# Optimization experiments

Hardware: AMD Instinct MI355X
Metric: run time of the kernel (lower is better)

Reference implementation:

```python
import jax, jax.numpy as jnp
import numpy as np

B, DIM1, DIM2, LATENT, T = 16, 1024, 1024, 512, 2048  # T == video_feat_dim
LN_EPS = 1e-5


def setup_inputs() -> dict:
    key = jax.random.key(0)
    ks = jax.random.split(key, 8)
    def xavier(k, shape):
        fan_out, fan_in = shape
        std = float(np.sqrt(2.0 / (fan_in + fan_out)))
        return jax.random.normal(k, shape, dtype=jnp.float32) * std
    return {
        "input1": jax.random.normal(ks[0], (B, DIM1, T), dtype=jnp.float32),
        "input2": jax.random.normal(ks[1], (B, DIM2, T), dtype=jnp.float32),
        "theta_w": xavier(ks[2], (LATENT, DIM2)),
        "theta_b": jnp.zeros((LATENT,), jnp.float32),
        "phi_w": xavier(ks[3], (LATENT, DIM1)),
        "phi_b": jnp.zeros((LATENT,), jnp.float32),
        "g_w": xavier(ks[4], (LATENT, DIM1)),
        "g_b": jnp.zeros((LATENT,), jnp.float32),
        "ln_gamma": jnp.ones((LATENT, T), jnp.float32),
        "ln_beta": jnp.zeros((LATENT, T), jnp.float32),
        "out_w": xavier(ks[5], (DIM2, LATENT)),
        "out_b": jnp.zeros((DIM2,), jnp.float32),
    }


def reference(input1, input2, theta_w, theta_b, phi_w, phi_b, g_w, g_b,
              ln_gamma, ln_beta, out_w, out_b):
    # 1x1 Conv1d == channel-wise matmul
    theta_x = jnp.einsum('ld,bdt->btl', theta_w, input2) + theta_b          # [B,T2,L]
    phi_x = jnp.einsum('ld,bdt->blt', phi_w, input1) + phi_b[:, None]       # [B,L,T1]
    scores = jnp.einsum('btl,bls->bts', theta_x, phi_x)                      # [B,T2,T1] (unscaled)
    p = jax.nn.softmax(scores, axis=-1)
    g_x = jnp.einsum('ld,bdt->btl', g_w, input1) + g_b                       # [B,T1,L]
    t_x = jnp.einsum('bts,bsl->blt', p, g_x)                                 # [B,L,T2]
    # LayerNorm over the last two dims jointly [LATENT, T]
    mu = jnp.mean(t_x, axis=(1, 2), keepdims=True)
    var = jnp.var(t_x, axis=(1, 2), keepdims=True)
    h = (t_x - mu) * jax.lax.rsqrt(var + LN_EPS) * ln_gamma + ln_beta
    h = jax.nn.relu(h)
    w_t = jnp.einsum('ol,blt->bot', out_w, h) + out_b[None, :, None]         # [B,DIM2,T2]
    return w_t + input2
```

## Files before the change

### kernel.cpp

```cpp
#include <hip/hip_runtime.h>
#include <hip/hip_bf16.h>

#define BB 16
#define D1 1024
#define D2 1024
#define LL 512
#define TT 2048
#define LN_EPS 1e-5f

typedef unsigned short u16;
typedef __attribute__((ext_vector_type(8))) _Float16 half8;
typedef __attribute__((ext_vector_type(4))) float f32x4;
typedef __attribute__((ext_vector_type(4))) unsigned int u32x4;

__device__ __forceinline__ u16 f2h(float v) {
    _Float16 h = (_Float16)v;
    return *(u16*)&h;
}
__device__ __forceinline__ float h2f(u16 u) {
    return (float)(*(const _Float16*)&u);
}

__device__ __forceinline__ void gload_lds16(const void* g, void* l) {
    __builtin_amdgcn_global_load_lds((const __attribute__((address_space(1))) void*)g,
                                     (__attribute__((address_space(3))) void*)l, 16, 0, 0);
}

#define MEMFENCE asm volatile("" ::: "memory")
__device__ __forceinline__ void block_barrier() {
    MEMFENCE; __builtin_amdgcn_s_barrier(); MEMFENCE;
}

template<int BIAS, int OMODE>
__global__ __launch_bounds__(512, 1) void nt_gemm(
    const u16* __restrict__ A, const u16* __restrict__ B,
    long sAb, long sBb, long sCb,
    int N, int Kd, int gx, int gy,
    const float* __restrict__ bias,
    void* __restrict__ out0,
    const float* __restrict__ resid, long sRb)
{
    __shared__ __align__(16) u16 smem[65536];

    const int nwg = gridDim.x;
    const int id = blockIdx.x;
    const int swz = (id & 7) * (nwg >> 3) + (id >> 3);
    const int bx = swz % gx;
    const int byz = swz / gx;
    const int by = byz % gy;
    const int b = byz / gy;

    const int tid = threadIdx.x;
    const long arow0 = (long)by * 256;
    const long brow0 = (long)bx * 256;
    const u16* Ab = A + (long)b * sAb + arow0 * Kd;
    const u16* Bb = B + (long)b * sBb + brow0 * Kd;

    const int wave = tid >> 6, lane = tid & 63;
    const int mh = wave >> 2;
    const int wm = mh * 128;
    const int wn = (wave & 3) * 64;
    const int lm = lane & 15, kg = lane >> 4;

    const int ntile = Kd >> 6;

    auto STAGE = [&](int buf, long k0) {
        u16* Ad = smem + buf * 32768;
        u16* Bd = Ad + 16384;
#pragma unroll
        for (int sw = 0; sw < 4; ++sw) {
            int idx = sw * 512 + tid;
            int m = idx >> 3, s = idx & 7;
            int gs = s ^ (m & 7);
            gload_lds16(Ab + k0 + (long)m * Kd + gs * 8, Ad + idx * 8);
        }
#pragma unroll
        for (int sw = 0; sw < 4; ++sw) {
            int idx = sw * 512 + tid;
            int m = idx >> 3, s = idx & 7;
            int gs = s ^ (m & 7);
            gload_lds16(Bb + k0 + (long)m * Kd + gs * 8, Bd + idx * 8);
        }
    };

    f32x4 acc[8][4];
#pragma unroll
    for (int i = 0; i < 8; ++i)
#pragma unroll
        for (int j = 0; j < 4; ++j) acc[i][j] = (f32x4){0.f, 0.f, 0.f, 0.f};

    STAGE(0, 0);
    if (ntile > 1) STAGE(1, 64);

    half8 a_[4][2], b_[2][2];

#define LOADA(ms_) do { \
    _Pragma("unroll") for (int f = 0; f < 4; ++f) \
    _Pragma("unroll") for (int kf = 0; kf < 2; ++kf) { \
        int mr = wm + (ms_) * 64 + f * 16 + lm; \
        int ss = (kf * 4 + kg) ^ (mr & 7); \
        a_[f][kf] = *(const half8*)(Ac + mr * 64 + ss * 8); } } while (0)
#define LOADB(ns_) do { \
    _Pragma("unroll") for (int f = 0; f < 2; ++f) \
    _Pragma("unroll") for (int kf = 0; kf < 2; ++kf) { \
        int nr = wn + (ns_) * 32 + f * 16 + lm; \
        int ss = (kf * 4 + kg) ^ (nr & 7); \
        b_[f][kf] = *(const half8*)(Bc + nr * 64 + ss * 8); } } while (0)
#define PH_MFMA(ms_, ns_) do { \
    block_barrier(); \
    asm volatile("s_waitcnt lgkmcnt(0)" ::: "memory"); \
    __builtin_amdgcn_sched_barrier(0); \
    __builtin_amdgcn_s_setprio(1); \
    _Pragma("unroll") for (int i = 0; i < 4; ++i) \
    _Pragma("unroll") for (int j = 0; j < 2; ++j) \
    _Pragma("unroll") for (int kf = 0; kf < 2; ++kf) \
        acc[(ms_) * 4 + i][(ns_) * 2 + j] = __builtin_amdgcn_mfma_f32_16x16x32_f16( \
            a_[i][kf], b_[j][kf], acc[(ms_) * 4 + i][(ns_) * 2 + j], 0, 0, 0); \
    __builtin_amdgcn_s_setprio(0); \
    block_barrier(); \
} while (0)

    for (int t = 0; t < ntile; ++t) {
        const int c = t & 1;
        const u16* Ac = smem + c * 32768;
        const u16* Bc = Ac + 16384;
        if (t + 1 < ntile) { asm volatile("s_waitcnt vmcnt(8)" ::: "memory"); }
        else               { asm volatile("s_waitcnt vmcnt(0)" ::: "memory"); }
        block_barrier();

        LOADA(0); LOADB(0); PH_MFMA(0, 0);
        LOADA(1);           PH_MFMA(1, 0);
        LOADB(1);           PH_MFMA(1, 1);
        LOADA(0);           PH_MFMA(0, 1);

        if (t + 2 < ntile) STAGE(c, (long)(t + 2) * 64);
    }
#undef LOADA
#undef LOADB
#undef PH_MFMA

    float* Cs = (float*)smem;
#pragma unroll
    for (int p = 0; p < 2; ++p) {
        __syncthreads();
        if (mh == p) {
#pragma unroll
            for (int ms = 0; ms < 2; ++ms)
#pragma unroll
                for (int i = 0; i < 4; ++i)
#pragma unroll
                    for (int ns = 0; ns < 2; ++ns)
#pragma unroll
                        for (int j = 0; j < 2; ++j)
#pragma unroll
                            for (int r = 0; r < 4; ++r) {
                                int row = ms * 64 + i * 16 + kg * 4 + r;
                                int col = wn + ns * 32 + j * 16 + lm;
                                Cs[row * 256 + (col ^ ((row & 7) << 2))] = acc[ms * 4 + i][ns * 2 + j][r];
                            }
        }
        __syncthreads();
        if (OMODE == 0 || OMODE == 3) {
#pragma unroll
            for (int it = 0; it < 16; ++it) {
                int elem = it * 512 + tid;
                int row = elem >> 6, c4 = elem & 63;
                int grow = (int)arow0 + p * 128 + row;
                int gcol = (int)brow0 + c4 * 4;
                f32x4 v = *(const f32x4*)&Cs[row * 256 + ((c4 ^ (row & 7)) << 2)];
                if (BIAS == 1) v += bias[grow];
                if (BIAS == 2) v += *(const f32x4*)(bias + gcol);
                long off = (long)b * sCb + (long)grow * N + gcol;
                if (OMODE == 3) {
                    f32x4 rv = __builtin_nontemporal_load(
                        (const f32x4*)(resid + (long)b * sRb + (long)grow * N + gcol));
                    v += rv;
                    __builtin_nontemporal_store(v, (f32x4*)((float*)out0 + off));
                } else {
                    *(f32x4*)((float*)out0 + off) = v;
                }
            }
        } else {
#pragma unroll
            for (int it = 0; it < 8; ++it) {
                int elem = it * 512 + tid;
                int row = elem >> 5, c8 = elem & 31;
                int grow = (int)arow0 + p * 128 + row;
                int gcol = (int)brow0 + c8 * 8;
                int g0 = (c8 * 2) ^ (row & 7);
                int g1 = (c8 * 2 + 1) ^ (row & 7);
                f32x4 u0 = *(const f32x4*)&Cs[row * 256 + g0 * 4];
                f32x4 u1 = *(const f32x4*)&Cs[row * 256 + g1 * 4];
                float vv[8] = {u0.x, u0.y, u0.z, u0.w, u1.x, u1.y, u1.z, u1.w};
                if (BIAS == 1) {
                    float bb = bias[grow];
#pragma unroll
                    for (int q = 0; q < 8; ++q) vv[q] += bb;
                }
                if (BIAS == 2) {
#pragma unroll
                    for (int q = 0; q < 8; ++q) vv[q] += bias[gcol + q];
                }
                union { u16 u[8]; u32x4 v4; } pk;
#pragma unroll
                for (int q = 0; q < 8; ++q) pk.u[q] = f2h(vv[q]);
                long off = (long)b * sCb + (long)grow * N + gcol;
                *(u32x4*)((u16*)out0 + off) = pk.v4;
            }
        }
    }
}

__device__ __forceinline__ void stage_tile_sm(const u16* __restrict__ g, int ldk, u16* lds, int tid) {
#pragma unroll
    for (int it = 0; it < 4; ++it) {
        int idx = it * 256 + tid;
        int m = idx >> 3, s = idx & 7;
        int gs = s ^ (m & 7);
        gload_lds16(g + (long)m * ldk + gs * 8, lds + idx * 8);
    }
}

template<int BIAS, int OMODE>
__global__ __launch_bounds__(256, 4) void nt_gemm_sm(
    const u16* __restrict__ A, const u16* __restrict__ B,
    long sAb, long sBb, long sCb,
    int N, int Kd, int gx, int gy,
    const float* __restrict__ bias,
    void* __restrict__ out0,
    const float* __restrict__ resid, long sRb)
{
    __shared__ __align__(16) u16 smem[2 * 128 * 64];
    u16* As = smem;
    u16* Bs = smem + 128 * 64;

    const int nwg = gridDim.x;
    const int id = blockIdx.x;
    const int swz = (id & 7) * (nwg >> 3) + (id >> 3);
    const int bx = swz % gx;
    const int byz = swz / gx;
    const int by = byz % gy;
    const int b = byz / gy;

    const int tid = threadIdx.x;
    const long arow0 = (long)by * 128;
    const long brow0 = (long)bx * 128;
    const u16* Ab = A + (long)b * sAb + arow0 * Kd;
    const u16* Bb = B + (long)b * sBb + brow0 * Kd;

    const int wave = tid >> 6, lane = tid & 63;
    const int wm = (wave >> 1) * 64, wn = (wave & 1) * 64;
    const int lm = lane & 15, kg = lane >> 4;

    f32x4 acc[4][4];
#pragma unroll
    for (int i = 0; i < 4; ++i)
#pragma unroll
        for (int j = 0; j < 4; ++j) acc[i][j] = (f32x4){0.f, 0.f, 0.f, 0.f};

    for (int k0 = 0; k0 < Kd; k0 += 64) {
        stage_tile_sm(Ab + k0, Kd, As, tid);
        stage_tile_sm(Bb + k0, Kd, Bs, tid);
        __syncthreads();
#pragma unroll
        for (int ks = 0; ks < 2; ++ks) {
            half8 af[4], bf[4];
#pragma unroll
            for (int f = 0; f < 4; ++f) {
                int mr = wm + f * 16 + lm;
                int as_ = (ks * 4 + kg) ^ (mr & 7);
                af[f] = *(const half8*)(As + mr * 64 + as_ * 8);
                int nr = wn + f * 16 + lm;
                int bs_ = (ks * 4 + kg) ^ (nr & 7);
                bf[f] = *(const half8*)(Bs + nr * 64 + bs_ * 8);
            }
#pragma unroll
            for (int i = 0; i < 4; ++i)
#pragma unroll
                for (int j = 0; j < 4; ++j)
                    acc[i][j] = __builtin_amdgcn_mfma_f32_16x16x32_f16(af[i], bf[j], acc[i][j], 0, 0, 0);
        }
        __syncthreads();
    }

    float* Cs = (float*)smem;
#pragma unroll
    for (int p = 0; p < 2; ++p) {
        if (p) __syncthreads();
        if (wm == p * 64) {
#pragma unroll
            for (int i = 0; i < 4; ++i)
#pragma unroll
                for (int j = 0; j < 4; ++j)
#pragma unroll
                    for (int r = 0; r < 4; ++r) {
                        int row = i * 16 + kg * 4 + r;
                        int col = wn + j * 16 + lm;
                        Cs[row * 128 + (col ^ ((row & 7) << 2))] = acc[i][j][r];
                    }
        }
        __syncthreads();
        if (OMODE == 0 || OMODE == 3) {
#pragma unroll
            for (int rr = 0; rr < 8; ++rr) {
                int elem = rr * 256 + tid;
                int row = elem >> 5, c4 = elem & 31;
                int grow = (int)arow0 + p * 64 + row;
                int gcol = (int)brow0 + c4 * 4;
                f32x4 v = *(const f32x4*)&Cs[row * 128 + ((c4 ^ (row & 7)) << 2)];
                if (BIAS == 1) v += bias[grow];
                if (BIAS == 2) v += *(const f32x4*)(bias + gcol);
                long off = (long)b * sCb + (long)grow * N + gcol;
                if (OMODE == 3) {
                    f32x4 rv = __builtin_nontemporal_load(
                        (const f32x4*)(resid + (long)b * sRb + (long)grow * N + gcol));
                    v += rv;
                    __builtin_nontemporal_store(v, (f32x4*)((float*)out0 + off));
                } else {
                    *(f32x4*)((float*)out0 + off) = v;
                }
            }
        } else {
#pragma unroll
            for (int rr = 0; rr < 4; ++rr) {
                int elem = rr * 256 + tid;
                int row = elem >> 4, c8 = elem & 15;
                int grow = (int)arow0 + p * 64 + row;
                int gcol = (int)brow0 + c8 * 8;
                int g0 = (c8 * 2) ^ (row & 7);
                int g1 = (c8 * 2 + 1) ^ (row & 7);
                f32x4 u0 = *(const f32x4*)&Cs[row * 128 + g0 * 4];
                f32x4 u1 = *(const f32x4*)&Cs[row * 128 + g1 * 4];
                float vv[8] = {u0.x, u0.y, u0.z, u0.w, u1.x, u1.y, u1.z, u1.w};
                if (BIAS == 1) {
                    float bb = bias[grow];
#pragma unroll
                    for (int q = 0; q < 8; ++q) vv[q] += bb;
                }
                if (BIAS == 2) {
#pragma unroll
                    for (int q = 0; q < 8; ++q) vv[q] += bias[gcol + q];
                }
                union { u16 u[8]; u32x4 v4; } pk;
#pragma unroll
                for (int q = 0; q < 8; ++q) pk.u[q] = f2h(vv[q]);
                long off = (long)b * sCb + (long)grow * N + gcol;
                *(u32x4*)((u16*)out0 + off) = pk.v4;
            }
        }
    }
}

__global__ __launch_bounds__(256) void transpose_h(const float* __restrict__ in,
                                                   u16* __restrict__ o16, int D, int T) {
    __shared__ float tile[64][65];
    int b = blockIdx.z;
    const float* src = in + (long)b * D * T;
    long obase = (long)b * D * T;
    int t0 = blockIdx.x * 64, d0 = blockIdx.y * 64;
    int tx = threadIdx.x & 63, ty = threadIdx.x >> 6;
#pragma unroll
    for (int i = 0; i < 64; i += 4)
        tile[ty + i][tx] = __builtin_nontemporal_load(&src[(long)(d0 + ty + i) * T + t0 + tx]);
    __syncthreads();
#pragma unroll
    for (int i = 0; i < 64; i += 4) {
        long o = obase + (long)(t0 + ty + i) * D + d0 + tx;
        o16[o] = f2h(tile[tx][ty + i]);
    }
}

__global__ __launch_bounds__(256) void transpose_f32(const float* __restrict__ in,
                                                     float* __restrict__ out, int R, int C) {
    __shared__ float tile[64][65];
    int c0 = blockIdx.x * 64, r0 = blockIdx.y * 64;
    int tx = threadIdx.x & 63, ty = threadIdx.x >> 6;
#pragma unroll
    for (int i = 0; i < 64; i += 4)
        tile[ty + i][tx] = in[(long)(r0 + ty + i) * C + c0 + tx];
    __syncthreads();
#pragma unroll
    for (int i = 0; i < 64; i += 4)
        out[(long)(c0 + ty + i) * R + r0 + tx] = tile[tx][ty + i];
}

__global__ __launch_bounds__(256) void conv_w(const float* __restrict__ w,
                                              u16* __restrict__ h, int n) {
    int i = blockIdx.x * 256 + threadIdx.x;
    if (i < n) h[i] = f2h(w[i]);
}

__global__ __launch_bounds__(256) void softmax_rows(const float* __restrict__ S, u16* __restrict__ P) {
    long row = (long)blockIdx.z * TT + blockIdx.x;
    const float* s = S + row * TT;
    u16* p = P + row * TT;
    int tid = threadIdx.x;
    f32x4 v0 = *(const f32x4*)(s + tid * 8);
    f32x4 v1 = *(const f32x4*)(s + tid * 8 + 4);
    float x[8] = {v0.x, v0.y, v0.z, v0.w, v1.x, v1.y, v1.z, v1.w};
    float m = x[0];
#pragma unroll
    for (int j = 1; j < 8; ++j) m = fmaxf(m, x[j]);
#pragma unroll
    for (int off = 32; off; off >>= 1) m = fmaxf(m, __shfl_xor(m, off, 64));
    __shared__ float red[8];
    int wave = tid >> 6, lane = tid & 63;
    if (lane == 0) red[wave] = m;
    __syncthreads();
    m = fmaxf(fmaxf(red[0], red[1]), fmaxf(red[2], red[3]));
    float e[8]; float sum = 0.f;
#pragma unroll
    for (int j = 0; j < 8; ++j) { e[j] = __expf(x[j] - m); sum += e[j]; }
#pragma unroll
    for (int off = 32; off; off >>= 1) sum += __shfl_xor(sum, off, 64);
    if (lane == 0) red[4 + wave] = sum;
    __syncthreads();
    sum = red[4] + red[5] + red[6] + red[7];
    float inv = 1.f / sum;
    union { u16 u[8]; u32x4 v4; } pk;
#pragma unroll
    for (int j = 0; j < 8; ++j) pk.u[j] = f2h(e[j] * inv);
    *(u32x4*)(p + tid * 8) = pk.v4;
}

__global__ void zero32(float* p) { p[threadIdx.x] = 0.f; }

__global__ __launch_bounds__(256) void ln_partial(const u16* __restrict__ TXp, float* __restrict__ sums) {
    int b = blockIdx.z;
    const u16* x = TXp + (long)b * (LL * TT) + (long)blockIdx.x * 32768;
    int tid = threadIdx.x;
    float s = 0.f, sq = 0.f;
#pragma unroll 4
    for (int j = 0; j < 16; ++j) {
        u32x4 v = *(const u32x4*)(x + (j * 256 + tid) * 8);
        unsigned w[4] = {v.x, v.y, v.z, v.w};
#pragma unroll
        for (int q = 0; q < 4; ++q) {
            float a = h2f((u16)(w[q] & 0xffff));
            float c = h2f((u16)(w[q] >> 16));
            s += a + c;
            sq += a * a + c * c;
        }
    }
#pragma unroll
    for (int off = 32; off; off >>= 1) { s += __shfl_xor(s, off, 64); sq += __shfl_xor(sq, off, 64); }
    __shared__ float rs[8];
    int wave = tid >> 6, lane = tid & 63;
    if (lane == 0) { rs[wave] = s; rs[4 + wave] = sq; }
    __syncthreads();
    if (tid == 0) {
        atomicAdd(&sums[b * 2], rs[0] + rs[1] + rs[2] + rs[3]);
        atomicAdd(&sums[b * 2 + 1], rs[4] + rs[5] + rs[6] + rs[7]);
    }
}

__global__ __launch_bounds__(256) void ln_apply(const u16* __restrict__ TXp, const float* __restrict__ sums,
                                                const float* __restrict__ gT, const float* __restrict__ bT,
                                                u16* __restrict__ H) {
    int b = blockIdx.z;
    const float n = (float)(LL * TT);
    float mu = sums[b * 2] / n;
    float var = sums[b * 2 + 1] / n - mu * mu;
    float rstd = rsqrtf(var + LN_EPS);
    long base = (long)b * (LL * TT);
    long idx = ((long)blockIdx.x * 256 + threadIdx.x) * 8;
    u32x4 xv = *(const u32x4*)(TXp + base + idx);
    unsigned w[4] = {xv.x, xv.y, xv.z, xv.w};
    f32x4 g0 = *(const f32x4*)(gT + idx);
    f32x4 g1 = *(const f32x4*)(gT + idx + 4);
    f32x4 b0 = *(const f32x4*)(bT + idx);
    f32x4 b1 = *(const f32x4*)(bT + idx + 4);
    float g[8] = {g0.x, g0.y, g0.z, g0.w, g1.x, g1.y, g1.z, g1.w};
    float be[8] = {b0.x, b0.y, b0.z, b0.w, b1.x, b1.y, b1.z, b1.w};
    union { u16 u[8]; u32x4 v; } pk;
#pragma unroll
    for (int q = 0; q < 4; ++q) {
        float a = h2f((u16)(w[q] & 0xffff));
        float c = h2f((u16)(w[q] >> 16));
        float oa = fmaxf((a - mu) * rstd * g[q * 2] + be[q * 2], 0.f);
        float oc = fmaxf((c - mu) * rstd * g[q * 2 + 1] + be[q * 2 + 1], 0.f);
        pk.u[q * 2] = f2h(oa);
        pk.u[q * 2 + 1] = f2h(oc);
    }
    *(u32x4*)(H + base + idx) = pk.v;
}

extern "C" void kernel_launch(void* const* d_in, const int* in_sizes, int n_in,
                              void* d_out, int out_size, void* d_ws, size_t ws_size,
                              hipStream_t stream) {
    const float* input1  = (const float*)d_in[0];
    const float* input2  = (const float*)d_in[1];
    const float* theta_w = (const float*)d_in[2];
    const float* theta_b = (const float*)d_in[3];
    const float* phi_w   = (const float*)d_in[4];
    const float* phi_b   = (const float*)d_in[5];
    const float* g_w     = (const float*)d_in[6];
    const float* g_b     = (const float*)d_in[7];
    const float* ln_gamma= (const float*)d_in[8];
    const float* ln_beta = (const float*)d_in[9];
    const float* out_w   = (const float*)d_in[10];
    const float* out_b   = (const float*)d_in[11];
    float* out = (float*)d_out;

    char* ws = (char*)d_ws;
    const size_t MB = 1ull << 20;
    u16*  Xt     = (u16*)(ws + 0);
    float* scores= (float*)(ws + 0);
    u16*  pmat   = (u16*)(ws + 64 * MB);
    u16*  Qf     = (u16*)(ws + 96 * MB);
    u16*  Kf     = (u16*)(ws + 128 * MB);
    u16*  Vt     = (u16*)(ws + 160 * MB);
    u16*  TX     = (u16*)(ws + 192 * MB);
    u16*  H      = (u16*)(ws + 224 * MB);
    u16*  thw    = (u16*)(ws + 256 * MB);
    u16*  phw    = (u16*)(ws + 257 * MB);
    u16*  gww    = (u16*)(ws + 258 * MB);
    u16*  oww    = (u16*)(ws + 259 * MB);
    float* gammaT= (float*)(ws + 260 * MB);
    float* betaT = (float*)(ws + 264 * MB);
    float* sums  = (float*)(ws + 268 * MB);

    dim3 blk(256), blk5(512);

    conv_w<<<dim3((LL * D2 + 255) / 256), blk, 0, stream>>>(theta_w, thw, LL * D2);
    conv_w<<<dim3((LL * D1 + 255) / 256), blk, 0, stream>>>(phi_w, phw, LL * D1);
    conv_w<<<dim3((LL * D1 + 255) / 256), blk, 0, stream>>>(g_w, gww, LL * D1);
    conv_w<<<dim3((D2 * LL + 255) / 256), blk, 0, stream>>>(out_w, oww, D2 * LL);
    transpose_f32<<<dim3(TT / 64, LL / 64, 1), blk, 0, stream>>>(ln_gamma, gammaT, LL, TT);
    transpose_f32<<<dim3(TT / 64, LL / 64, 1), blk, 0, stream>>>(ln_beta, betaT, LL, TT);

    transpose_h<<<dim3(TT / 64, D2 / 64, BB), blk, 0, stream>>>(input2, Xt, D2, TT);
    nt_gemm_sm<2, 1><<<dim3((LL / 128) * (TT / 128) * BB), blk, 0, stream>>>(
        Xt, thw, (long)TT * D2, 0, (long)TT * LL, LL, D2, LL / 128, TT / 128,
        theta_b, Qf, nullptr, 0);

    transpose_h<<<dim3(TT / 64, D1 / 64, BB), blk, 0, stream>>>(input1, Xt, D1, TT);
    nt_gemm_sm<2, 1><<<dim3((LL / 128) * (TT / 128) * BB), blk, 0, stream>>>(
        Xt, phw, (long)TT * D1, 0, (long)TT * LL, LL, D1, LL / 128, TT / 128,
        phi_b, Kf, nullptr, 0);
    nt_gemm_sm<1, 1><<<dim3((TT / 128) * (LL / 128) * BB), blk, 0, stream>>>(
        gww, Xt, 0, (long)TT * D1, (long)LL * TT, TT, D1, TT / 128, LL / 128,
        g_b, Vt, nullptr, 0);

    for (int c = 0; c < 4; ++c) {
        long qoff = (long)c * 4 * TT * LL;
        nt_gemm<0, 0><<<dim3((TT / 256) * (TT / 256) * 4), blk5, 0, stream>>>(
            Qf + qoff, Kf + qoff, (long)TT * LL, (long)TT * LL, (long)TT * TT,
            TT, LL, TT / 256, TT / 256, nullptr, scores, nullptr, 0);
        softmax_rows<<<dim3(TT, 1, 4), blk, 0, stream>>>(scores, pmat);
        nt_gemm_sm<0, 1><<<dim3((LL / 128) * (TT / 128) * 4), blk, 0, stream>>>(
            pmat, Vt + (long)c * 4 * LL * TT, (long)TT * TT, (long)LL * TT, (long)TT * LL,
            LL, TT, LL / 128, TT / 128, nullptr, TX + qoff, nullptr, 0);
    }

    zero32<<<dim3(1), dim3(32), 0, stream>>>(sums);
    ln_partial<<<dim3(32, 1, BB), blk, 0, stream>>>(TX, sums);
    ln_apply<<<dim3(512, 1, BB), blk, 0, stream>>>(TX, sums, gammaT, betaT, H);

    nt_gemm_sm<1, 3><<<dim3((TT / 128) * (D2 / 128) * BB), blk, 0, stream>>>(
        oww, H, 0, (long)TT * LL, (long)D2 * TT, TT, LL, TT / 128, D2 / 128,
        out_b, out, input2, (long)D2 * TT);
}
```

Baseline: 638.4 us.

## Use 256-tile GEMM for projections, restructure its main loop, fuse LN stats into PV GEMM

Result: no change. 628.0 us (-1.6%).

```diff
diff --git a/kernel.cpp b/kernel.cpp
--- a/kernel.cpp
+++ b/kernel.cpp
@@ -32,7 +32,7 @@
 }
 
 template<int BIAS, int OMODE>
-__global__ __launch_bounds__(512, 1) void nt_gemm(
+__global__ __launch_bounds__(512, 2) void nt_gemm(
     const u16* __restrict__ A, const u16* __restrict__ B,
     long sAb, long sBb, long sCb,
     int N, int Kd, int gx, int gy,
@@ -57,29 +57,26 @@
     const u16* Bb = B + (long)b * sBb + brow0 * Kd;
 
     const int wave = tid >> 6, lane = tid & 63;
-    const int mh = wave >> 2;
-    const int wm = mh * 128;
-    const int wn = (wave & 3) * 64;
+    const int wm = (wave >> 2) * 128, wn = (wave & 3) * 64;
     const int lm = lane & 15, kg = lane >> 4;
 
-    const int ntile = Kd >> 6;
+    const int m0 = tid >> 3, s0 = tid & 7;
+    const int nt = Kd >> 6;
 
     auto STAGE = [&](int buf, long k0) {
         u16* Ad = smem + buf * 32768;
-        u16* Bd = Ad + 16384;
-#pragma unroll
-        for (int sw = 0; sw < 4; ++sw) {
-            int idx = sw * 512 + tid;
-            int m = idx >> 3, s = idx & 7;
-            int gs = s ^ (m & 7);
-            gload_lds16(Ab + k0 + (long)m * Kd + gs * 8, Ad + idx * 8);
-        }
-#pragma unroll
-        for (int sw = 0; sw < 4; ++sw) {
-            int idx = sw * 512 + tid;
-            int m = idx >> 3, s = idx & 7;
-            int gs = s ^ (m & 7);
-            gload_lds16(Bb + k0 + (long)m * Kd + gs * 8, Bd + idx * 8);
+        u16* Bd = smem + buf * 32768 + 16384;
+#pragma unroll
+        for (int call = 0; call < 4; ++call) {
+            int m = call * 64 + m0;
+            int gs = s0 ^ (m & 7);
+            gload_lds16(Ab + k0 + (long)m * Kd + gs * 8, Ad + (call * 512 + tid) * 8);
+        }
+#pragma unroll
+        for (int call = 0; call < 4; ++call) {
+            int m = call * 64 + m0;
+            int gs = s0 ^ (m & 7);
+            gload_lds16(Bb + k0 + (long)m * Kd + gs * 8, Bd + (call * 512 + tid) * 8);
         }
     };
 
@@ -90,74 +87,67 @@
         for (int j = 0; j < 4; ++j) acc[i][j] = (f32x4){0.f, 0.f, 0.f, 0.f};
 
     STAGE(0, 0);
-    if (ntile > 1) STAGE(1, 64);
-
-    half8 a_[4][2], b_[2][2];
-
-#define LOADA(ms_) do { \
-    _Pragma("unroll") for (int f = 0; f < 4; ++f) \
-    _Pragma("unroll") for (int kf = 0; kf < 2; ++kf) { \
-        int mr = wm + (ms_) * 64 + f * 16 + lm; \
-        int ss = (kf * 4 + kg) ^ (mr & 7); \
-        a_[f][kf] = *(const half8*)(Ac + mr * 64 + ss * 8); } } while (0)
-#define LOADB(ns_) do { \
-    _Pragma("unroll") for (int f = 0; f < 2; ++f) \
-    _Pragma("unroll") for (int kf = 0; kf < 2; ++kf) { \
-        int nr = wn + (ns_) * 32 + f * 16 + lm; \
-        int ss = (kf * 4 + kg) ^ (nr & 7); \
-        b_[f][kf] = *(const half8*)(Bc + nr * 64 + ss * 8); } } while (0)
-#define PH_MFMA(ms_, ns_) do { \
-    block_barrier(); \
-    asm volatile("s_waitcnt lgkmcnt(0)" ::: "memory"); \
-    __builtin_amdgcn_sched_barrier(0); \
-    __builtin_amdgcn_s_setprio(1); \
-    _Pragma("unroll") for (int i = 0; i < 4; ++i) \
-    _Pragma("unroll") for (int j = 0; j < 2; ++j) \
-    _Pragma("unroll") for (int kf = 0; kf < 2; ++kf) \
-        acc[(ms_) * 4 + i][(ns_) * 2 + j] = __builtin_amdgcn_mfma_f32_16x16x32_f16( \
-            a_[i][kf], b_[j][kf], acc[(ms_) * 4 + i][(ns_) * 2 + j], 0, 0, 0); \
-    __builtin_amdgcn_s_setprio(0); \
-    block_barrier(); \
-} while (0)
-
-    for (int t = 0; t < ntile; ++t) {
-        const int c = t & 1;
-        const u16* Ac = smem + c * 32768;
-        const u16* Bc = Ac + 16384;
-        if (t + 1 < ntile) { asm volatile("s_waitcnt vmcnt(8)" ::: "memory"); }
-        else               { asm volatile("s_waitcnt vmcnt(0)" ::: "memory"); }
+    if (nt > 1) STAGE(1, 64);
+
+    for (int t = 0; t < nt; ++t) {
+        const int cur = t & 1;
+        if (t + 1 < nt) { asm volatile("s_waitcnt vmcnt(8)" ::: "memory"); }
+        else           { asm volatile("s_waitcnt vmcnt(0)" ::: "memory"); }
         block_barrier();
 
-        LOADA(0); LOADB(0); PH_MFMA(0, 0);
-        LOADA(1);           PH_MFMA(1, 0);
-        LOADB(1);           PH_MFMA(1, 1);
-        LOADA(0);           PH_MFMA(0, 1);
-
-        if (t + 2 < ntile) STAGE(c, (long)(t + 2) * 64);
-    }
-#undef LOADA
-#undef LOADB
-#undef PH_MFMA
+        const u16* Ac = smem + cur * 32768;
+        const u16* Bc = smem + cur * 32768 + 16384;
+
+        half8 bf[4][2];
+#pragma unroll
+        for (int f = 0; f < 4; ++f)
+#pragma unroll
+            for (int kf = 0; kf < 2; ++kf) {
+                int nr = wn + f * 16 + lm;
+                int ss = (kf * 4 + kg) ^ (nr & 7);
+                bf[f][kf] = *(const half8*)(Bc + nr * 64 + ss * 8);
+            }
+#pragma unroll
+        for (int mh = 0; mh < 2; ++mh) {
+            half8 af[4][2];
+#pragma unroll
+            for (int f = 0; f < 4; ++f)
+#pragma unroll
+                for (int kf = 0; kf < 2; ++kf) {
+                    int mr = wm + mh * 64 + f * 16 + lm;
+                    int ss = (kf * 4 + kg) ^ (mr & 7);
+                    af[f][kf] = *(const half8*)(Ac + mr * 64 + ss * 8);
+                }
+            __builtin_amdgcn_s_setprio(1);
+#pragma unroll
+            for (int f = 0; f < 4; ++f)
+#pragma unroll
+                for (int j = 0; j < 4; ++j)
+#pragma unroll
+                    for (int kf = 0; kf < 2; ++kf)
+                        acc[mh * 4 + f][j] = __builtin_amdgcn_mfma_f32_16x16x32_f16(
+                            af[f][kf], bf[j][kf], acc[mh * 4 + f][j], 0, 0, 0);
+            __builtin_amdgcn_s_setprio(0);
+        }
+        block_barrier();
+        if (t + 2 < nt) STAGE(cur, (long)(t + 2) * 64);
+    }
 
     float* Cs = (float*)smem;
 #pragma unroll
     for (int p = 0; p < 2; ++p) {
         __syncthreads();
-        if (mh == p) {
-#pragma unroll
-            for (int ms = 0; ms < 2; ++ms)
-#pragma unroll
-                for (int i = 0; i < 4; ++i)
-#pragma unroll
-                    for (int ns = 0; ns < 2; ++ns)
-#pragma unroll
-                        for (int j = 0; j < 2; ++j)
-#pragma unroll
-                            for (int r = 0; r < 4; ++r) {
-                                int row = ms * 64 + i * 16 + kg * 4 + r;
-                                int col = wn + ns * 32 + j * 16 + lm;
-                                Cs[row * 256 + (col ^ ((row & 7) << 2))] = acc[ms * 4 + i][ns * 2 + j][r];
-                            }
+        if (wm == p * 128) {
+#pragma unroll
+            for (int i = 0; i < 8; ++i)
+#pragma unroll
+                for (int j = 0; j < 4; ++j)
+#pragma unroll
+                    for (int r = 0; r < 4; ++r) {
+                        int row = i * 16 + kg * 4 + r;
+                        int col = wn + j * 16 + lm;
+                        Cs[row * 256 + (col ^ ((row & 7) << 2))] = acc[i][j][r];
+                    }
         }
         __syncthreads();
         if (OMODE == 0 || OMODE == 3) {
@@ -221,14 +211,15 @@
     }
 }
 
-template<int BIAS, int OMODE>
+template<int BIAS, int OMODE, int LNS>
 __global__ __launch_bounds__(256, 4) void nt_gemm_sm(
     const u16* __restrict__ A, const u16* __restrict__ B,
     long sAb, long sBb, long sCb,
     int N, int Kd, int gx, int gy,
     const float* __restrict__ bias,
     void* __restrict__ out0,
-    const float* __restrict__ resid, long sRb)
+    const float* __restrict__ resid, long sRb,
+    float* __restrict__ lnsums)
 {
     __shared__ __align__(16) u16 smem[2 * 128 * 64];
     u16* As = smem;
@@ -283,6 +274,7 @@
         __syncthreads();
     }
 
+    float ls = 0.f, lsq = 0.f;
     float* Cs = (float*)smem;
 #pragma unroll
     for (int p = 0; p < 2; ++p) {
@@ -341,12 +333,30 @@
 #pragma unroll
                     for (int q = 0; q < 8; ++q) vv[q] += bias[gcol + q];
                 }
+                if (LNS) {
+#pragma unroll
+                    for (int q = 0; q < 8; ++q) { ls += vv[q]; lsq += vv[q] * vv[q]; }
+                }
                 union { u16 u[8]; u32x4 v4; } pk;
 #pragma unroll
                 for (int q = 0; q < 8; ++q) pk.u[q] = f2h(vv[q]);
                 long off = (long)b * sCb + (long)grow * N + gcol;
                 *(u32x4*)((u16*)out0 + off) = pk.v4;
             }
+        }
+    }
+    if (LNS) {
+#pragma unroll
+        for (int off = 32; off; off >>= 1) {
+            ls += __shfl_xor(ls, off, 64);
+            lsq += __shfl_xor(lsq, off, 64);
+        }
+        __shared__ float rsum[8];
+        if (lane == 0) { rsum[wave] = ls; rsum[4 + wave] = lsq; }
+        __syncthreads();
+        if (tid == 0) {
+            atomicAdd(&lnsums[b * 2], rsum[0] + rsum[1] + rsum[2] + rsum[3]);
+            atomicAdd(&lnsums[b * 2 + 1], rsum[4] + rsum[5] + rsum[6] + rsum[7]);
         }
     }
 }
@@ -424,35 +434,6 @@
 }
 
 __global__ void zero32(float* p) { p[threadIdx.x] = 0.f; }
-
-__global__ __launch_bounds__(256) void ln_partial(const u16* __restrict__ TXp, float* __restrict__ sums) {
-    int b = blockIdx.z;
-    const u16* x = TXp + (long)b * (LL * TT) + (long)blockIdx.x * 32768;
-    int tid = threadIdx.x;
-    float s = 0.f, sq = 0.f;
-#pragma unroll 4
-    for (int j = 0; j < 16; ++j) {
-        u32x4 v = *(const u32x4*)(x + (j * 256 + tid) * 8);
-        unsigned w[4] = {v.x, v.y, v.z, v.w};
-#pragma unroll
-        for (int q = 0; q < 4; ++q) {
-            float a = h2f((u16)(w[q] & 0xffff));
-            float c = h2f((u16)(w[q] >> 16));
-            s += a + c;
-            sq += a * a + c * c;
-        }
-    }
-#pragma unroll
-    for (int off = 32; off; off >>= 1) { s += __shfl_xor(s, off, 64); sq += __shfl_xor(sq, off, 64); }
-    __shared__ float rs[8];
-    int wave = tid >> 6, lane = tid & 63;
-    if (lane == 0) { rs[wave] = s; rs[4 + wave] = sq; }
-    __syncthreads();
-    if (tid == 0) {
-        atomicAdd(&sums[b * 2], rs[0] + rs[1] + rs[2] + rs[3]);
-        atomicAdd(&sums[b * 2 + 1], rs[4] + rs[5] + rs[6] + rs[7]);
-    }
-}
 
 __global__ __launch_bounds__(256) void ln_apply(const u16* __restrict__ TXp, const float* __restrict__ sums,
                                                 const float* __restrict__ gT, const float* __restrict__ bT,
@@ -528,18 +509,19 @@
     conv_w<<<dim3((D2 * LL + 255) / 256), blk, 0, stream>>>(out_w, oww, D2 * LL);
     transpose_f32<<<dim3(TT / 64, LL / 64, 1), blk, 0, stream>>>(ln_gamma, gammaT, LL, TT);
     transpose_f32<<<dim3(TT / 64, LL / 64, 1), blk, 0, stream>>>(ln_beta, betaT, LL, TT);
+    zero32<<<dim3(1), dim3(32), 0, stream>>>(sums);
 
     transpose_h<<<dim3(TT / 64, D2 / 64, BB), blk, 0, stream>>>(input2, Xt, D2, TT);
-    nt_gemm_sm<2, 1><<<dim3((LL / 128) * (TT / 128) * BB), blk, 0, stream>>>(
-        Xt, thw, (long)TT * D2, 0, (long)TT * LL, LL, D2, LL / 128, TT / 128,
+    nt_gemm<2, 1><<<dim3((LL / 256) * (TT / 256) * BB), blk5, 0, stream>>>(
+        Xt, thw, (long)TT * D2, 0, (long)TT * LL, LL, D2, LL / 256, TT / 256,
         theta_b, Qf, nullptr, 0);
 
     transpose_h<<<dim3(TT / 64, D1 / 64, BB), blk, 0, stream>>>(input1, Xt, D1, TT);
-    nt_gemm_sm<2, 1><<<dim3((LL / 128) * (TT / 128) * BB), blk, 0, stream>>>(
-        Xt, phw, (long)TT * D1, 0, (long)TT * LL, LL, D1, LL / 128, TT / 128,
+    nt_gemm<2, 1><<<dim3((LL / 256) * (TT / 256) * BB), blk5, 0, stream>>>(
+        Xt, phw, (long)TT * D1, 0, (long)TT * LL, LL, D1, LL / 256, TT / 256,
         phi_b, Kf, nullptr, 0);
-    nt_gemm_sm<1, 1><<<dim3((TT / 128) * (LL / 128) * BB), blk, 0, stream>>>(
-        gww, Xt, 0, (long)TT * D1, (long)LL * TT, TT, D1, TT / 128, LL / 128,
+    nt_gemm<1, 1><<<dim3((TT / 256) * (LL / 256) * BB), blk5, 0, stream>>>(
+        gww, Xt, 0, (long)TT * D1, (long)LL * TT, TT, D1, TT / 256, LL / 256,
         g_b, Vt, nullptr, 0);
 
     for (int c = 0; c < 4; ++c) {
@@ -548,16 +530,14 @@
             Qf + qoff, Kf + qoff, (long)TT * LL, (long)TT * LL, (long)TT * TT,
             TT, LL, TT / 256, TT / 256, nullptr, scores, nullptr, 0);
         softmax_rows<<<dim3(TT, 1, 4), blk, 0, stream>>>(scores, pmat);
-        nt_gemm_sm<0, 1><<<dim3((LL / 128) * (TT / 128) * 4), blk, 0, stream>>>(
+        nt_gemm_sm<0, 1, 1><<<dim3((LL / 128) * (TT / 128) * 4), blk, 0, stream>>>(
             pmat, Vt + (long)c * 4 * LL * TT, (long)TT * TT, (long)LL * TT, (long)TT * LL,
-            LL, TT, LL / 128, TT / 128, nullptr, TX + qoff, nullptr, 0);
-    }
-
-    zero32<<<dim3(1), dim3(32), 0, stream>>>(sums);
-    ln_partial<<<dim3(32, 1, BB), blk, 0, stream>>>(TX, sums);
+            LL, TT, LL / 128, TT / 128, nullptr, TX + qoff, nullptr, 0, sums + (long)c * 8);
+    }
+
     ln_apply<<<dim3(512, 1, BB), blk, 0, stream>>>(TX, sums, gammaT, betaT, H);
 
-    nt_gemm_sm<1, 3><<<dim3((TT / 128) * (D2 / 128) * BB), blk, 0, stream>>>(
+    nt_gemm_sm<1, 3, 0><<<dim3((TT / 128) * (D2 / 128) * BB), blk, 0, stream>>>(
         oww, H, 0, (long)TT * LL, (long)D2 * TT, TT, LL, TT / 128, D2 / 128,
-        out_b, out, input2, (long)D2 * TT);
-}
+        out_b, out, input2, (long)D2 * TT, nullptr);
+}
```
